# Kernel optimization log

Hardware: AMD Instinct MI355X
Metric: run time of the kernel (lower is better)

Reference implementation:

```python
import jax, jax.numpy as jnp
import numpy as np

C = 16          # scalar multiplicity of Rs_hidden = [(16, 0)]
NB = 10         # number_of_basis
H = 12          # radial MLP hidden size
MAX_R = 10.0
CENTERS = jnp.linspace(0.0, MAX_R, NB)
SIGMA = 0.8 * (MAX_R / (NB - 1))
GAUSS_NORM = 1.423085244900308   # e3nn GaussianRadialModel basis normalizer
Y0 = 1.0 / (2.0 * np.sqrt(np.pi))  # Y_{l=0} spherical harmonic constant


def setup_inputs() -> dict:
    key = jax.random.key(0)
    ks = jax.random.split(key, 9)
    z, n1, n2 = 4, 192, 192
    return {
        'input1': jax.random.normal(ks[0], (z, n1, C), jnp.float32),
        'input2': jax.random.normal(ks[1], (z, n2, C), jnp.float32),
        'xyz1': jax.random.normal(ks[2], (z, n1, 3), jnp.float32),
        'xyz2': jax.random.normal(ks[3], (z, n2, 3), jnp.float32),
        'mask': jax.random.randint(ks[4], (z, n1 + n2), 0, 2),
        'W_rad1': jax.random.normal(ks[5], (NB, H), jnp.float32),
        'W_rad_out': jax.random.normal(ks[6], (H, C * C), jnp.float32),
        'W_fc3': jax.random.normal(ks[7], (C, C), jnp.float32),
        'W_fc2': jax.random.normal(ks[8], (C, 1), jnp.float32),
    }


def _normalize(x, eps=1e-6):
    # torch .std defaults to unbiased (ddof=1)
    mean = x.mean(-1, keepdims=True)
    std = jnp.std(x, axis=-1, keepdims=True, ddof=1)
    return (x - mean) / (std + eps)


def reference(input1, input2, xyz1, xyz2, mask, W_rad1, W_rad_out, W_fc3, W_fc2):
    x = jnp.concatenate([input1, input2], axis=1)    # [z, n, C]
    xyz = jnp.concatenate([xyz1, xyz2], axis=1)      # [z, n, 3]
    z, n = x.shape[0], x.shape[1]

    # pairwise distances (eps keeps sqrt grad finite on the diagonal)
    diff = xyz[:, :, None, :] - xyz[:, None, :, :]   # [z, n, n, 3]
    d = jnp.sqrt(jnp.sum(diff * diff, axis=-1) + 1e-12)  # [z, n, n]

    # Gaussian radial basis + weight-normalized FC radial model (swish act)
    basis = jnp.exp(-jnp.square((d[..., None] - CENTERS) / SIGMA)) / GAUSS_NORM  # [z,n,n,NB]
    hmid = jax.nn.silu(basis @ W_rad1 / np.sqrt(NB))          # [z, n, n, H]
    R = hmid @ W_rad_out / np.sqrt(H)                         # [z, n, n, C*C]

    # l=0 TFN kernel: radial weights * Y_0 (trivial Clebsch-Gordan for scalars)
    K = R.reshape(z, n, n, C, C) * Y0                         # [z, a, b, i, j]
    y = jnp.einsum('zabij,zbj->zai', K, x)                    # [z, n, C]

    # Norm(Rs_hidden): per-irrep L2 norm; for scalars it's |x|
    y = jnp.abs(y)
    y = jnp.where(mask[..., None] == 0, 0.0, y)

    s = _normalize(jnp.sum(y, axis=1))                        # [z, C]
    h3 = jax.nn.leaky_relu(s @ W_fc3 / np.sqrt(C))            # fc3 + leaky_relu
    o = h3 @ W_fc2 / np.sqrt(C)                               # fc2
    return jax.nn.sigmoid(o).reshape(-1)                      # [z]
```

## Files before the change

### kernel.cpp

```cpp
#include <hip/hip_runtime.h>
#include <math.h>

#define Z     4
#define N1    192
#define NN    384
#define C     16
#define NB    10
#define H     12
#define ATILE 4
#define NAT   (NN / ATILE)
#define SPLIT 6

__device__ __forceinline__ float fexp2(float x) {
    float r; asm volatile("v_exp_f32 %0, %1" : "=v"(r) : "v"(x)); return r;
}
__device__ __forceinline__ float frcp(float x) {
    float r; asm volatile("v_rcp_f32 %0, %1" : "=v"(r) : "v"(x)); return r;
}

__device__ __forceinline__ float3 load_xyz(const float* __restrict__ xyz1,
                                           const float* __restrict__ xyz2,
                                           int z, int node) {
    const float* p = (node < N1) ? (xyz1 + (z * N1 + node) * 3)
                                 : (xyz2 + (z * N1 + (node - N1)) * 3);
    return make_float3(p[0], p[1], p[2]);
}

__global__ void k1_precompute_T(const float* __restrict__ in1,
                                const float* __restrict__ in2,
                                const float* __restrict__ Wro,
                                float* __restrict__ T,
                                float* __restrict__ y_acc) {
    const int bid = blockIdx.x;
    const int z = bid / NN, b = bid % NN;
    const int t = threadIdx.x;

    __shared__ float xl[C];
    if (t < C) {
        const float* xp = (b < N1) ? (in1 + (z * N1 + b) * C)
                                   : (in2 + (z * N1 + (b - N1)) * C);
        xl[t] = xp[t];
    }
    if (bid < 128) y_acc[bid * 192 + t] = 0.0f;
    __syncthreads();

    const int h = t >> 4, i = t & 15;
    const float* w = Wro + h * (C * C) + i * C;
    float acc = 0.0f;
    #pragma unroll
    for (int j = 0; j < C; ++j) acc += w[j] * xl[j];

    const float scale = 0.28209479177387814f * 0.2886751345948129f;
    T[((z * H + h) * C + i) * NN + b] = acc * scale;
}

__global__ __launch_bounds__(64) void k2_pairs(const float* __restrict__ xyz1,
                                               const float* __restrict__ xyz2,
                                               const float* __restrict__ Wr1,
                                               const float* __restrict__ T,
                                               float* __restrict__ y_acc) {
    const int bid = blockIdx.x;
    const int sp  = bid % SPLIT;
    const int za  = bid / SPLIT;
    const int z   = za / NAT, at = za % NAT;
    const int a0  = at * ATILE;
    const int lane = threadIdx.x;
    const int b = sp * 64 + lane;

    __shared__ float W1s[NB * H];
    for (int idx = lane; idx < NB * H; idx += 64)
        W1s[idx] = Wr1[idx] * (0.31622776601683794f * 0.7027283689263438f);
    __syncthreads();

    const float3 pb = load_xyz(xyz1, xyz2, z, b);

    float dd[ATILE];
    #pragma unroll
    for (int aa = 0; aa < ATILE; ++aa) {
        const float3 pa = load_xyz(xyz1, xyz2, z, a0 + aa);
        const float dx = pa.x - pb.x, dy = pa.y - pb.y, dz = pa.z - pb.z;
        dd[aa] = sqrtf(dx * dx + dy * dy + dz * dz + 1e-12f);
    }

    float hm[ATILE][H];
    #pragma unroll
    for (int aa = 0; aa < ATILE; ++aa)
        #pragma unroll
        for (int h = 0; h < H; ++h) hm[aa][h] = 0.0f;

    #pragma unroll
    for (int k = 0; k < NB; ++k) {
        const float4 w0 = *(const float4*)&W1s[k * H + 0];
        const float4 w1 = *(const float4*)&W1s[k * H + 4];
        const float4 w2 = *(const float4*)&W1s[k * H + 8];
        const float ck = (float)k * (10.0f / 9.0f);
        #pragma unroll
        for (int aa = 0; aa < ATILE; ++aa) {
            const float t = dd[aa] - ck;
            const float e = fexp2(t * t * -1.8259109111250943f);
            hm[aa][0]  += e * w0.x;  hm[aa][1]  += e * w0.y;
            hm[aa][2]  += e * w0.z;  hm[aa][3]  += e * w0.w;
            hm[aa][4]  += e * w1.x;  hm[aa][5]  += e * w1.y;
            hm[aa][6]  += e * w1.z;  hm[aa][7]  += e * w1.w;
            hm[aa][8]  += e * w2.x;  hm[aa][9]  += e * w2.y;
            hm[aa][10] += e * w2.z;  hm[aa][11] += e * w2.w;
        }
    }
    #pragma unroll
    for (int aa = 0; aa < ATILE; ++aa)
        #pragma unroll
        for (int h = 0; h < H; ++h) {
            const float x = hm[aa][h];
            const float sig = frcp(1.0f + fexp2(x * -1.4426950408889634f));
            hm[aa][h] = x * sig;
        }

    float v[ATILE * C];
    #pragma unroll
    for (int p = 0; p < ATILE * C; ++p) v[p] = 0.0f;

    const float* tb = T + (z * H * C) * NN + b;
    #pragma unroll
    for (int h = 0; h < H; ++h) {
        #pragma unroll
        for (int i = 0; i < C; ++i) {
            const float tval = tb[(h * C + i) * NN];
            #pragma unroll
            for (int aa = 0; aa < ATILE; ++aa)
                v[aa * C + i] += hm[aa][h] * tval;
        }
    }

    #pragma unroll
    for (int k = 0; k < 6; ++k) {
        const int m = 32 >> k;
        const int bsel = (lane >> k) & 1;
        #pragma unroll
        for (int j = 0; j < m; ++j) {
            const float lo = v[j], hi = v[m + j];
            const float sendv = bsel ? lo : hi;
            const float recv = __shfl_xor(sendv, 1 << k, 64);
            v[j] = (bsel ? hi : lo) + recv;
        }
    }
    const int l = lane;
    const int pos = ((l & 1) << 5) | ((l & 2) << 3) | ((l & 4) << 1) |
                    ((l & 8) >> 1) | ((l & 16) >> 3) | ((l & 32) >> 5);
    atomicAdd(&y_acc[(z * NN + a0) * C + pos], v[0]);
}

__global__ __launch_bounds__(256) void k3_head(const float* __restrict__ y_acc,
                                               const int* __restrict__ mask,
                                               const float* __restrict__ Wfc3,
                                               const float* __restrict__ Wfc2,
                                               float* __restrict__ out) {
    const int z = blockIdx.x;
    const int t = threadIdx.x;
    const int i = t & 15, ch = t >> 4;

    __shared__ float red[16][17];

    float acc = 0.0f;
    #pragma unroll
    for (int r = 0; r < 24; ++r) {
        const int a = ch * 24 + r;
        const float val = y_acc[(z * NN + a) * C + i];
        if (mask[z * NN + a] != 0) acc += fabsf(val);
    }
    red[ch][i] = acc;
    __syncthreads();

    if (t < C) {
        float x = 0.0f;
        #pragma unroll
        for (int c2 = 0; c2 < 16; ++c2) x += red[c2][t];

        float m = x;
        #pragma unroll
        for (int msk = 1; msk < 16; msk <<= 1) m += __shfl_xor(m, msk, 64);
        m *= (1.0f / 16.0f);
        const float dv = x - m;
        float vv = dv * dv;
        #pragma unroll
        for (int msk = 1; msk < 16; msk <<= 1) vv += __shfl_xor(vv, msk, 64);
        const float sd = sqrtf(vv / 15.0f) + 1e-6f;
        const float xn = dv / sd;

        float h3 = 0.0f;
        #pragma unroll
        for (int q = 0; q < 16; ++q)
            h3 += __shfl(xn, q, 64) * Wfc3[q * C + t];
        h3 *= 0.25f;
        h3 = (h3 > 0.0f) ? h3 : 0.01f * h3;

        float o = h3 * Wfc2[t];
        #pragma unroll
        for (int msk = 1; msk < 16; msk <<= 1) o += __shfl_xor(o, msk, 64);
        if (t == 0) out[z] = 1.0f / (1.0f + __expf(-0.25f * o));
    }
}

extern "C" void kernel_launch(void* const* d_in, const int* in_sizes, int n_in,
                              void* d_out, int out_size, void* d_ws, size_t ws_size,
                              hipStream_t stream) {
    const float* in1  = (const float*)d_in[0];
    const float* in2  = (const float*)d_in[1];
    const float* xyz1 = (const float*)d_in[2];
    const float* xyz2 = (const float*)d_in[3];
    const int*   mask = (const int*)d_in[4];
    const float* Wr1  = (const float*)d_in[5];
    const float* Wro  = (const float*)d_in[6];
    const float* Wfc3 = (const float*)d_in[7];
    const float* Wfc2 = (const float*)d_in[8];
    float* out = (float*)d_out;

    float* T     = (float*)d_ws;
    float* y_acc = T + Z * NN * H * C;

    k1_precompute_T<<<Z * NN, 192, 0, stream>>>(in1, in2, Wro, T, y_acc);
    k2_pairs<<<Z * NAT * SPLIT, 64, 0, stream>>>(xyz1, xyz2, Wr1, T, y_acc);
    k3_head<<<Z, 256, 0, stream>>>(y_acc, mask, Wfc3, Wfc2, out);
}
```

Baseline: 95.45 us.

## Fuse head reduction into pair kernel via last-block counter

```diff
diff --git a/kernel.cpp b/kernel.cpp
--- a/kernel.cpp
+++ b/kernel.cpp
@@ -10,6 +10,7 @@
 #define ATILE 4
 #define NAT   (NN / ATILE)
 #define SPLIT 6
+#define GRID2 (Z * NAT * SPLIT)
 
 __device__ __forceinline__ float fexp2(float x) {
     float r; asm volatile("v_exp_f32 %0, %1" : "=v"(r) : "v"(x)); return r;
@@ -26,39 +27,48 @@
     return make_float3(p[0], p[1], p[2]);
 }
 
-__global__ void k1_precompute_T(const float* __restrict__ in1,
-                                const float* __restrict__ in2,
-                                const float* __restrict__ Wro,
-                                float* __restrict__ T,
-                                float* __restrict__ y_acc) {
-    const int bid = blockIdx.x;
-    const int z = bid / NN, b = bid % NN;
-    const int t = threadIdx.x;
-
-    __shared__ float xl[C];
-    if (t < C) {
-        const float* xp = (b < N1) ? (in1 + (z * N1 + b) * C)
-                                   : (in2 + (z * N1 + (b - N1)) * C);
-        xl[t] = xp[t];
-    }
-    if (bid < 128) y_acc[bid * 192 + t] = 0.0f;
-    __syncthreads();
-
-    const int h = t >> 4, i = t & 15;
+__global__ __launch_bounds__(384) void k1_precompute_T(const float* __restrict__ in1,
+                                                       const float* __restrict__ in2,
+                                                       const float* __restrict__ Wro,
+                                                       float* __restrict__ T,
+                                                       float* __restrict__ y_acc,
+                                                       unsigned int* __restrict__ counter) {
+    const int row = blockIdx.x;
+    const int b   = threadIdx.x;
+    const int z   = row / (H * C);
+    const int hi  = row % (H * C);
+    const int h   = hi >> 4, i = hi & 15;
+
+    if (row < 64) y_acc[row * 384 + b] = 0.0f;
+    if (row == 0 && b == 0) *counter = 0u;
+
+    const float* xp = (b < N1) ? (in1 + (z * N1 + b) * C)
+                               : (in2 + (z * N1 + (b - N1)) * C);
     const float* w = Wro + h * (C * C) + i * C;
+    const float4 x0 = *(const float4*)(xp + 0);
+    const float4 x1 = *(const float4*)(xp + 4);
+    const float4 x2 = *(const float4*)(xp + 8);
+    const float4 x3 = *(const float4*)(xp + 12);
     float acc = 0.0f;
-    #pragma unroll
-    for (int j = 0; j < C; ++j) acc += w[j] * xl[j];
+    acc += w[0]  * x0.x + w[1]  * x0.y + w[2]  * x0.z + w[3]  * x0.w;
+    acc += w[4]  * x1.x + w[5]  * x1.y + w[6]  * x1.z + w[7]  * x1.w;
+    acc += w[8]  * x2.x + w[9]  * x2.y + w[10] * x2.z + w[11] * x2.w;
+    acc += w[12] * x3.x + w[13] * x3.y + w[14] * x3.z + w[15] * x3.w;
 
     const float scale = 0.28209479177387814f * 0.2886751345948129f;
-    T[((z * H + h) * C + i) * NN + b] = acc * scale;
+    T[row * NN + b] = acc * scale;
 }
 
 __global__ __launch_bounds__(64) void k2_pairs(const float* __restrict__ xyz1,
                                                const float* __restrict__ xyz2,
+                                               const int* __restrict__ mask,
                                                const float* __restrict__ Wr1,
+                                               const float* __restrict__ Wfc3,
+                                               const float* __restrict__ Wfc2,
                                                const float* __restrict__ T,
-                                               float* __restrict__ y_acc) {
+                                               float* __restrict__ y_acc,
+                                               unsigned int* __restrict__ counter,
+                                               float* __restrict__ out) {
     const int bid = blockIdx.x;
     const int sp  = bid % SPLIT;
     const int za  = bid / SPLIT;
@@ -147,33 +157,27 @@
     const int pos = ((l & 1) << 5) | ((l & 2) << 3) | ((l & 4) << 1) |
                     ((l & 8) >> 1) | ((l & 16) >> 3) | ((l & 32) >> 5);
     atomicAdd(&y_acc[(z * NN + a0) * C + pos], v[0]);
-}
-
-__global__ __launch_bounds__(256) void k3_head(const float* __restrict__ y_acc,
-                                               const int* __restrict__ mask,
-                                               const float* __restrict__ Wfc3,
-                                               const float* __restrict__ Wfc2,
-                                               float* __restrict__ out) {
-    const int z = blockIdx.x;
-    const int t = threadIdx.x;
-    const int i = t & 15, ch = t >> 4;
-
-    __shared__ float red[16][17];
-
-    float acc = 0.0f;
-    #pragma unroll
-    for (int r = 0; r < 24; ++r) {
-        const int a = ch * 24 + r;
-        const float val = y_acc[(z * NN + a) * C + i];
-        if (mask[z * NN + a] != 0) acc += fabsf(val);
-    }
-    red[ch][i] = acc;
-    __syncthreads();
-
-    if (t < C) {
-        float x = 0.0f;
-        #pragma unroll
-        for (int c2 = 0; c2 < 16; ++c2) x += red[c2][t];
+
+    __threadfence();
+    unsigned int old = 0;
+    if (lane == 0) old = atomicAdd(counter, 1u);
+    old = (unsigned int)__shfl((int)old, 0, 64);
+    if (old != GRID2 - 1) return;
+    __threadfence();
+
+    const int ch = lane >> 4;
+    const int i  = lane & 15;
+    #pragma unroll
+    for (int zz = 0; zz < Z; ++zz) {
+        float acc = 0.0f;
+        for (int r = 0; r < 96; ++r) {
+            const int a = ch * 96 + r;
+            const float val = y_acc[(zz * NN + a) * C + i];
+            if (mask[zz * NN + a] != 0) acc += fabsf(val);
+        }
+        acc += __shfl_xor(acc, 16, 64);
+        acc += __shfl_xor(acc, 32, 64);
+        const float x = acc;
 
         float m = x;
         #pragma unroll
@@ -189,14 +193,14 @@
         float h3 = 0.0f;
         #pragma unroll
         for (int q = 0; q < 16; ++q)
-            h3 += __shfl(xn, q, 64) * Wfc3[q * C + t];
+            h3 += __shfl(xn, q, 64) * Wfc3[q * C + i];
         h3 *= 0.25f;
         h3 = (h3 > 0.0f) ? h3 : 0.01f * h3;
 
-        float o = h3 * Wfc2[t];
+        float o = h3 * Wfc2[i];
         #pragma unroll
         for (int msk = 1; msk < 16; msk <<= 1) o += __shfl_xor(o, msk, 64);
-        if (t == 0) out[z] = 1.0f / (1.0f + __expf(-0.25f * o));
+        if (lane == 0) out[zz] = 1.0f / (1.0f + __expf(-0.25f * o));
     }
 }
 
@@ -216,8 +220,9 @@
 
     float* T     = (float*)d_ws;
     float* y_acc = T + Z * NN * H * C;
-
-    k1_precompute_T<<<Z * NN, 192, 0, stream>>>(in1, in2, Wro, T, y_acc);
-    k2_pairs<<<Z * NAT * SPLIT, 64, 0, stream>>>(xyz1, xyz2, Wr1, T, y_acc);
-    k3_head<<<Z, 256, 0, stream>>>(y_acc, mask, Wfc3, Wfc2, out);
-}
+    unsigned int* counter = (unsigned int*)(y_acc + Z * NN * C);
+
+    k1_precompute_T<<<Z * H * C, 384, 0, stream>>>(in1, in2, Wro, T, y_acc, counter);
+    k2_pairs<<<GRID2, 64, 0, stream>>>(xyz1, xyz2, mask, Wr1, Wfc3, Wfc2,
+                                       T, y_acc, counter, out);
+}
```

Result: slower. 234.4 us (+145.6%).
